# Kernel tuning notes

Measured on AMD Instinct MI355X. Metric: run time of the kernel, lower is better.

The kernel has to match this reference:

```python
import jax, jax.numpy as jnp
import numpy as np

N_HEAD = 12
NEG_INF = -10000.0


def setup_inputs() -> dict:
    key = jax.random.key(0)
    k1, k2, k3 = jax.random.split(key, 3)
    B, S, D = 8, 1024, 768
    std = 0.01
    return {
        "hidden_states": jax.random.normal(k1, (B, S, D), dtype=jnp.float32),
        "Wqkv": jax.random.normal(k2, (D, 3 * D), dtype=jnp.float32) * std,
        "bqkv": jnp.zeros((3 * D,), dtype=jnp.float32),
        "Wout": jax.random.normal(k3, (D, D), dtype=jnp.float32) * std,
        "bout": jnp.zeros((D,), dtype=jnp.float32),
    }


def reference(hidden_states, Wqkv, bqkv, Wout, bout):
    B, S, D = hidden_states.shape
    H = N_HEAD
    hd = D // H
    # fused QKV projection
    qkv = hidden_states @ Wqkv + bqkv  # [B,S,3D]
    qkv = qkv.reshape(B, S, 3, H, hd)
    q, k, v = qkv[:, :, 0], qkv[:, :, 1], qkv[:, :, 2]  # [B,S,H,hd]
    q = q.transpose(0, 2, 1, 3)  # [B,H,S,hd]
    k = k.transpose(0, 2, 1, 3)
    v = v.transpose(0, 2, 1, 3)
    scale = 1.0 / jnp.sqrt(jnp.asarray(hd, dtype=hidden_states.dtype))
    scores = jnp.einsum("bhqd,bhkd->bhqk", q, k) * scale  # [B,H,S,S]
    causal = jnp.tril(jnp.ones((S, S), dtype=bool))[None, None]
    scores = jnp.where(causal, scores, jnp.asarray(NEG_INF, scores.dtype))
    probs = jax.nn.softmax(scores, axis=-1)
    # dropout is identity in eval/deterministic mode
    attn = jnp.einsum("bhqk,bhkd->bhqd", probs, v)  # [B,H,S,hd]
    attn = attn.transpose(0, 2, 1, 3).reshape(B, S, D)
    return attn @ Wout + bout
```

## Files before the change

### kernel.cpp

```cpp
#include <hip/hip_runtime.h>
#include <hip/hip_bf16.h>

#define B_   8
#define S_   1024
#define D_   768
#define H_   12
#define HD_  64
#define BS_  (B_*S_)
#define N3_  (3*D_)

typedef __attribute__((ext_vector_type(8))) short short8;
typedef __attribute__((ext_vector_type(4))) float f32x4;

__device__ __forceinline__ short8 ld8(const __hip_bfloat16* p) {
    return *reinterpret_cast<const short8*>(p);
}
__device__ __forceinline__ void st8(__hip_bfloat16* p, short8 v) {
    *reinterpret_cast<short8*>(p) = v;
}
__device__ __forceinline__ f32x4 mfma16(short8 a, short8 b, f32x4 c) {
    return __builtin_amdgcn_mfma_f32_16x16x32_bf16(a, b, c, 0, 0, 0);
}
__device__ __forceinline__ void async16(const __hip_bfloat16* g, __hip_bfloat16* l) {
    __builtin_amdgcn_global_load_lds((const __attribute__((address_space(1))) void*)g,
                                     (__attribute__((address_space(3))) void*)l,
                                     16, 0, 0);
}
__device__ __forceinline__ float fast_exp2(float x) {
#if __has_builtin(__builtin_amdgcn_exp2f)
    return __builtin_amdgcn_exp2f(x);
#else
    return __expf(x * 0.69314718056f);
#endif
}

__global__ void cast_f32_bf16(const float* __restrict__ in,
                              __hip_bfloat16* __restrict__ out, int n) {
    int i = (blockIdx.x * blockDim.x + threadIdx.x) * 4;
    if (i + 3 < n) {
        float4 v = *reinterpret_cast<const float4*>(in + i);
        out[i + 0] = __float2bfloat16(v.x);
        out[i + 1] = __float2bfloat16(v.y);
        out[i + 2] = __float2bfloat16(v.z);
        out[i + 3] = __float2bfloat16(v.w);
    }
}

__global__ void transpose_cast(const float* __restrict__ in,
                               __hip_bfloat16* __restrict__ out, int R, int C) {
    __shared__ float tile[32][33];
    int c0 = blockIdx.x * 32, r0 = blockIdx.y * 32;
    for (int i = threadIdx.y; i < 32; i += 8) {
        tile[i][threadIdx.x] = in[(size_t)(r0 + i) * C + c0 + threadIdx.x];
    }
    __syncthreads();
    for (int i = threadIdx.y; i < 32; i += 8) {
        out[(size_t)(c0 + i) * R + r0 + threadIdx.x] =
            __float2bfloat16(tile[threadIdx.x][i]);
    }
}

__global__ __launch_bounds__(256)
void gemm_qkv(const __hip_bfloat16* __restrict__ A,
              const __hip_bfloat16* __restrict__ Bt,
              const float* __restrict__ bqkv,
              __hip_bfloat16* __restrict__ Qb,
              __hip_bfloat16* __restrict__ Kb,
              __hip_bfloat16* __restrict__ Vtb) {
    __shared__ __align__(16) char smem[49152];
    __hip_bfloat16* Ct = (__hip_bfloat16*)smem;

    int tid = threadIdx.x, wave = tid >> 6, lane = tid & 63;
    int ln = lane & 15, quad = lane >> 4;
    int mb = blockIdx.y * 128, nb = blockIdx.x * 128;
    int wm = (wave >> 1) * 64, wn = (wave & 1) * 64;

    f32x4 acc[4][4];
#pragma unroll
    for (int i = 0; i < 4; ++i)
#pragma unroll
        for (int j = 0; j < 4; ++j) acc[i][j] = (f32x4){0.f, 0.f, 0.f, 0.f};

    auto stage = [&](int k, int bufoff) {
        __hip_bfloat16* Asb = (__hip_bfloat16*)(smem + bufoff);
        __hip_bfloat16* Bsb = Asb + 128 * 32;
#pragma unroll
        for (int it = 0; it < 2; ++it) {
            int c = it * 256 + tid;
            int row = c >> 2, cc = c & 3;
            int csw = cc ^ ((row >> 1) & 3);
            async16(A + (size_t)(mb + row) * D_ + k + csw * 8,
                    Asb + it * 2048 + wave * 512);
            async16(Bt + (size_t)(nb + row) * D_ + k + csw * 8,
                    Bsb + it * 2048 + wave * 512);
        }
    };

    auto compute = [&](int bufoff) {
        __hip_bfloat16* As = (__hip_bfloat16*)(smem + bufoff);
        __hip_bfloat16* Bs = As + 128 * 32;
        short8 a[4], b[4];
#pragma unroll
        for (int i = 0; i < 4; ++i) {
            int row = wm + i * 16 + ln;
            a[i] = ld8(As + row * 32 + ((quad ^ ((row >> 1) & 3)) << 3));
        }
#pragma unroll
        for (int j = 0; j < 4; ++j) {
            int row = wn + j * 16 + ln;
            b[j] = ld8(Bs + row * 32 + ((quad ^ ((row >> 1) & 3)) << 3));
        }
#pragma unroll
        for (int i = 0; i < 4; ++i)
#pragma unroll
            for (int j = 0; j < 4; ++j)
                acc[i][j] = mfma16(a[i], b[j], acc[i][j]);
    };

    stage(0, 0);
    stage(32, 16384);
    int cb = 0;
    for (int k = 0; k < D_ - 32; k += 32) {
        asm volatile("s_waitcnt vmcnt(4)" ::: "memory");
        asm volatile("s_barrier" ::: "memory");
        if (k + 64 < D_) {
            int sb = cb + 32768; if (sb >= 49152) sb -= 49152;
            stage(k + 64, sb);
        }
        compute(cb);
        cb += 16384; if (cb >= 49152) cb = 0;
    }
    asm volatile("s_waitcnt vmcnt(0)" ::: "memory");
    asm volatile("s_barrier" ::: "memory");
    compute(cb);
    __syncthreads();

    int which = blockIdx.x / 6;
    int nbr = nb - which * D_;
    float qscale = (which == 0) ? (0.125f * 1.44269504089f) : 1.f;

#pragma unroll
    for (int j = 0; j < 4; ++j) {
        int col = wn + j * 16 + ln;
        float bias = bqkv[nb + col];
#pragma unroll
        for (int i = 0; i < 4; ++i)
#pragma unroll
            for (int r = 0; r < 4; ++r) {
                int row = wm + i * 16 + quad * 4 + r;
                __hip_bfloat16 v = __float2bfloat16((acc[i][j][r] + bias) * qscale);
                if (which != 2) Ct[row * 132 + col] = v;
                else            Ct[col * 132 + row] = v;
            }
    }
    __syncthreads();

    int bb = mb >> 10, sb = mb & 1023;
    if (which != 2) {
        __hip_bfloat16* dst = (which == 0) ? Qb : Kb;
#pragma unroll
        for (int it = 0; it < 8; ++it) {
            int cc = it * 256 + tid;
            int row = cc >> 4, c8 = cc & 15;
            short8 v = ld8(Ct + row * 132 + c8 * 8);
            int gcol = nbr + c8 * 8;
            int h = gcol >> 6, d = gcol & 63;
            int s = sb + row;
            st8(dst + (((size_t)(bb * H_ + h)) * S_ + s) * HD_ + d, v);
        }
    } else {
#pragma unroll
        for (int it = 0; it < 8; ++it) {
            int cc = it * 256 + tid;
            int drow = cc >> 4, s8 = cc & 15;
            short8 v = ld8(Ct + drow * 132 + s8 * 8);
            int gd = nbr + drow;
            int h = gd >> 6, d = gd & 63;
            st8(Vtb + ((size_t)(bb * H_ + h) * HD_ + d) * S_ + sb + s8 * 8, v);
        }
    }
}

__global__ __launch_bounds__(256, 3)
void attn_flash3(const __hip_bfloat16* __restrict__ Q,
                 const __hip_bfloat16* __restrict__ K,
                 const __hip_bfloat16* __restrict__ Vt,
                 __hip_bfloat16* __restrict__ attnbf) {
    __shared__ __hip_bfloat16 Kbuf[2][64 * 64];
    __shared__ __hip_bfloat16 Vbuf[2][64 * 64];
    __shared__ __hip_bfloat16 Pbuf[4][32 * 72];

    int bh = blockIdx.y;
    int ip = blockIdx.x;
    int tid = threadIdx.x;
    int wave = tid >> 6, lane = tid & 63;
    int ln = lane & 15, quad = lane >> 4;
    int strip = (wave < 2) ? ip : (15 - ip);
    int qrow0 = strip * 64 + (wave & 1) * 32;

    const __hip_bfloat16* Qbh = Q + (size_t)bh * S_ * HD_;
    const __hip_bfloat16* Kbh = K + (size_t)bh * S_ * HD_;
    const __hip_bfloat16* Vbh = Vt + (size_t)bh * HD_ * S_;

    short8 aq[2][2];
#pragma unroll
    for (int rt = 0; rt < 2; ++rt)
#pragma unroll
        for (int ks = 0; ks < 2; ++ks)
            aq[rt][ks] = ld8(Qbh + (size_t)(qrow0 + rt * 16 + ln) * HD_ +
                             ks * 32 + quad * 8);

    f32x4 o[2][4];
    float l_run[2][4];
#pragma unroll
    for (int rt = 0; rt < 2; ++rt)
#pragma unroll
        for (int n = 0; n < 4; ++n) {
            o[rt][n] = (f32x4){0.f, 0.f, 0.f, 0.f};
            l_run[rt][n] = 0.f;
        }

    int last_kt = 15 - ip;

    auto stage = [&](int kt, int buf) {
        const __hip_bfloat16* gK = Kbh + (size_t)kt * 64 * HD_;
#pragma unroll
        for (int it = 0; it < 2; ++it) {
            int p = it * 256 + tid;
            int row = p >> 3;
            int csw = (p & 7) ^ (row & 7);
            async16(gK + row * HD_ + csw * 8,
                    &Kbuf[buf][it * 2048 + wave * 512]);
            async16(Vbh + (size_t)row * S_ + kt * 64 + csw * 8,
                    &Vbuf[buf][it * 2048 + wave * 512]);
        }
    };

    stage(0, 0);
    __syncthreads();
    int cur = 0;

    for (int kt = 0; kt <= last_kt; ++kt) {
        int kbase = kt * 64;
        if (kt < last_kt) stage(kt + 1, cur ^ 1);

        if (kbase <= qrow0 + 31) {
            const __hip_bfloat16* Kc = Kbuf[cur];
            const __hip_bfloat16* Vc = Vbuf[cur];

            f32x4 s[2][4];
#pragma unroll
            for (int rt = 0; rt < 2; ++rt)
#pragma unroll
                for (int j = 0; j < 4; ++j) s[rt][j] = (f32x4){0.f, 0.f, 0.f, 0.f};
#pragma unroll
            for (int j = 0; j < 4; ++j) {
                int row = j * 16 + ln;
#pragma unroll
                for (int ks = 0; ks < 2; ++ks) {
                    short8 bk = ld8(&Kc[row * 64 +
                                        (((ks * 4 + quad) ^ (row & 7)) << 3)]);
#pragma unroll
                    for (int rt = 0; rt < 2; ++rt)
                        s[rt][j] = mfma16(aq[rt][ks], bk, s[rt][j]);
                }
            }

            if (kbase + 63 > qrow0) {
#pragma unroll
                for (int rt = 0; rt < 2; ++rt)
#pragma unroll
                    for (int j = 0; j < 4; ++j) {
                        int key = kbase + j * 16 + ln;
#pragma unroll
                        for (int r = 0; r < 4; ++r) {
                            int q = qrow0 + rt * 16 + quad * 4 + r;
                            if (key > q) s[rt][j][r] = -INFINITY;
                        }
                    }
            }

#pragma unroll
            for (int rt = 0; rt < 2; ++rt)
#pragma unroll
                for (int j = 0; j < 4; ++j)
#pragma unroll
                    for (int r = 0; r < 4; ++r)
                        s[rt][j][r] = fast_exp2(s[rt][j][r]);
#pragma unroll
            for (int rt = 0; rt < 2; ++rt)
#pragma unroll
                for (int r = 0; r < 4; ++r)
                    l_run[rt][r] += (s[rt][0][r] + s[rt][1][r]) +
                                    (s[rt][2][r] + s[rt][3][r]);

#pragma unroll
            for (int rt = 0; rt < 2; ++rt)
#pragma unroll
                for (int j = 0; j < 4; ++j)
#pragma unroll
                    for (int r = 0; r < 4; ++r)
                        Pbuf[wave][(rt * 16 + quad * 4 + r) * 72 + j * 16 + ln] =
                            __float2bfloat16(s[rt][j][r]);
            asm volatile("s_waitcnt lgkmcnt(0)" ::: "memory");

            short8 ap[2][2];
#pragma unroll
            for (int rt = 0; rt < 2; ++rt)
#pragma unroll
                for (int ks = 0; ks < 2; ++ks)
                    ap[rt][ks] = ld8(&Pbuf[wave][(rt * 16 + ln) * 72 +
                                                 ks * 32 + quad * 8]);

#pragma unroll
            for (int n = 0; n < 4; ++n) {
                int row = n * 16 + ln;
#pragma unroll
                for (int ks = 0; ks < 2; ++ks) {
                    short8 bv = ld8(&Vc[row * 64 +
                                        (((ks * 4 + quad) ^ (row & 7)) << 3)]);
#pragma unroll
                    for (int rt = 0; rt < 2; ++rt)
                        o[rt][n] = mfma16(ap[rt][ks], bv, o[rt][n]);
                }
            }
        }

        __syncthreads();
        cur ^= 1;
    }

    int bb = bh / H_, h = bh - bb * H_;
#pragma unroll
    for (int rt = 0; rt < 2; ++rt)
#pragma unroll
        for (int r = 0; r < 4; ++r) {
            float l = l_run[rt][r];
            l += __shfl_xor(l, 1);
            l += __shfl_xor(l, 2);
            l += __shfl_xor(l, 4);
            l += __shfl_xor(l, 8);
            float inv = 1.f / l;
            int row = qrow0 + rt * 16 + quad * 4 + r;
#pragma unroll
            for (int n = 0; n < 4; ++n) {
                int col = h * 64 + n * 16 + ln;
                attnbf[((size_t)bb * S_ + row) * D_ + col] =
                    __float2bfloat16(o[rt][n][r] * inv);
            }
        }
}

__global__ __launch_bounds__(256)
void gemm_out(const __hip_bfloat16* __restrict__ A,
              const __hip_bfloat16* __restrict__ Bt,
              const float* __restrict__ bias,
              float* __restrict__ Cout) {
    __shared__ __align__(16) char smem[49152];

    int tid = threadIdx.x, wave = tid >> 6, lane = tid & 63;
    int ln = lane & 15, quad = lane >> 4;
    int mb = blockIdx.y * 128, nb = blockIdx.x * 128;
    int wm = (wave >> 1) * 64, wn = (wave & 1) * 64;

    f32x4 acc[4][4];
#pragma unroll
    for (int i = 0; i < 4; ++i)
#pragma unroll
        for (int j = 0; j < 4; ++j) acc[i][j] = (f32x4){0.f, 0.f, 0.f, 0.f};

    auto stage = [&](int k, int bufoff) {
        __hip_bfloat16* Asb = (__hip_bfloat16*)(smem + bufoff);
        __hip_bfloat16* Bsb = Asb + 128 * 32;
#pragma unroll
        for (int it = 0; it < 2; ++it) {
            int c = it * 256 + tid;
            int row = c >> 2, cc = c & 3;
            int csw = cc ^ ((row >> 1) & 3);
            async16(A + (size_t)(mb + row) * D_ + k + csw * 8,
                    Asb + it * 2048 + wave * 512);
            async16(Bt + (size_t)(nb + row) * D_ + k + csw * 8,
                    Bsb + it * 2048 + wave * 512);
        }
    };

    auto compute = [&](int bufoff) {
        __hip_bfloat16* As = (__hip_bfloat16*)(smem + bufoff);
        __hip_bfloat16* Bs = As + 128 * 32;
        short8 a[4], b[4];
#pragma unroll
        for (int i = 0; i < 4; ++i) {
            int row = wm + i * 16 + ln;
            a[i] = ld8(As + row * 32 + ((quad ^ ((row >> 1) & 3)) << 3));
        }
#pragma unroll
        for (int j = 0; j < 4; ++j) {
            int row = wn + j * 16 + ln;
            b[j] = ld8(Bs + row * 32 + ((quad ^ ((row >> 1) & 3)) << 3));
        }
#pragma unroll
        for (int i = 0; i < 4; ++i)
#pragma unroll
            for (int j = 0; j < 4; ++j)
                acc[i][j] = mfma16(a[i], b[j], acc[i][j]);
    };

    stage(0, 0);
    stage(32, 16384);
    int cb = 0;
    for (int k = 0; k < D_ - 32; k += 32) {
        asm volatile("s_waitcnt vmcnt(4)" ::: "memory");
        asm volatile("s_barrier" ::: "memory");
        if (k + 64 < D_) {
            int sb = cb + 32768; if (sb >= 49152) sb -= 49152;
            stage(k + 64, sb);
        }
        compute(cb);
        cb += 16384; if (cb >= 49152) cb = 0;
    }
    asm volatile("s_waitcnt vmcnt(0)" ::: "memory");
    asm volatile("s_barrier" ::: "memory");
    compute(cb);

#pragma unroll
    for (int j = 0; j < 4; ++j) {
        int col = nb + wn + j * 16 + ln;
        float bv = bias[col];
#pragma unroll
        for (int i = 0; i < 4; ++i)
#pragma unroll
            for (int r = 0; r < 4; ++r) {
                int row = mb + wm + i * 16 + quad * 4 + r;
                Cout[(size_t)row * D_ + col] = acc[i][j][r] + bv;
            }
    }
}

extern "C" void kernel_launch(void* const* d_in, const int* in_sizes, int n_in,
                              void* d_out, int out_size, void* d_ws, size_t ws_size,
                              hipStream_t stream) {
    const float* X    = (const float*)d_in[0];
    const float* Wqkv = (const float*)d_in[1];
    const float* bqkv = (const float*)d_in[2];
    const float* Wout = (const float*)d_in[3];
    const float* bout = (const float*)d_in[4];
    float* out = (float*)d_out;

    constexpr size_t SZ_XBF   = (size_t)BS_ * D_ * 2;
    constexpr size_t SZ_WQKVT = (size_t)N3_ * D_ * 2;
    constexpr size_t SZ_WOUTT = (size_t)D_ * D_ * 2;
    constexpr size_t SZ_QKV   = (size_t)B_ * H_ * S_ * HD_ * 2;

    char* w = (char*)d_ws;
    __hip_bfloat16* Xbf    = (__hip_bfloat16*)(w);
    __hip_bfloat16* WqkvT  = (__hip_bfloat16*)(w + SZ_XBF);
    __hip_bfloat16* WoutT  = (__hip_bfloat16*)(w + SZ_XBF + SZ_WQKVT);
    __hip_bfloat16* Qb     = (__hip_bfloat16*)(w + SZ_XBF + SZ_WQKVT + SZ_WOUTT);
    __hip_bfloat16* Kb     = (__hip_bfloat16*)(w + SZ_XBF + SZ_WQKVT + SZ_WOUTT + SZ_QKV);
    __hip_bfloat16* Vtb    = (__hip_bfloat16*)(w + SZ_XBF + SZ_WQKVT + SZ_WOUTT + 2*SZ_QKV);
    __hip_bfloat16* attnbf = (__hip_bfloat16*)(w + SZ_XBF + SZ_WQKVT + SZ_WOUTT + 3*SZ_QKV);
    (void)ws_size; (void)in_sizes; (void)n_in; (void)out_size;

    int nX = BS_ * D_;
    cast_f32_bf16<<<nX / (256 * 4), 256, 0, stream>>>(X, Xbf, nX);
    transpose_cast<<<dim3(N3_ / 32, D_ / 32), dim3(32, 8), 0, stream>>>(Wqkv, WqkvT, D_, N3_);
    transpose_cast<<<dim3(D_ / 32, D_ / 32), dim3(32, 8), 0, stream>>>(Wout, WoutT, D_, D_);

    gemm_qkv<<<dim3(N3_ / 128, BS_ / 128), 256, 0, stream>>>(Xbf, WqkvT, bqkv, Qb, Kb, Vtb);

    attn_flash3<<<dim3(8, B_ * H_), 256, 0, stream>>>(Qb, Kb, Vtb, attnbf);

    gemm_out<<<dim3(D_ / 128, BS_ / 128), 256, 0, stream>>>(attnbf, WoutT, bout, out);
}
```

Measured before the change: 191.1 us.

## Merge prep kernels, remap GEMM block order, narrow out-proj tile to 64 columns

Folds the X cast and both weight transposes into a single prep launch, removing two kernel launches and their gaps. Both GEMMs remap block indices so that consecutive launched blocks are spread across the M dimension in groups of 8, aiming for better cache or XCD locality. The output projection drops from 128x128 to 128x64 tiles, doubling its grid from 384 to 768 blocks so more CUs stay busy on MI355X, at the cost of lower per-block reuse. LDS buffering and the waitcnt values are adjusted to match.

```diff
diff --git a/kernel.cpp b/kernel.cpp
--- a/kernel.cpp
+++ b/kernel.cpp
@@ -34,30 +34,41 @@
 #endif
 }
 
-__global__ void cast_f32_bf16(const float* __restrict__ in,
-                              __hip_bfloat16* __restrict__ out, int n) {
-    int i = (blockIdx.x * blockDim.x + threadIdx.x) * 4;
-    if (i + 3 < n) {
-        float4 v = *reinterpret_cast<const float4*>(in + i);
-        out[i + 0] = __float2bfloat16(v.x);
-        out[i + 1] = __float2bfloat16(v.y);
-        out[i + 2] = __float2bfloat16(v.z);
-        out[i + 3] = __float2bfloat16(v.w);
-    }
-}
-
-__global__ void transpose_cast(const float* __restrict__ in,
-                               __hip_bfloat16* __restrict__ out, int R, int C) {
+#define PREP_CAST_BLK 6144
+#define PREP_WQKV_BLK 1728
+#define PREP_WOUT_BLK 576
+__global__ __launch_bounds__(256)
+void prep(const float* __restrict__ X, __hip_bfloat16* __restrict__ Xbf,
+          const float* __restrict__ Wqkv, __hip_bfloat16* __restrict__ WqkvT,
+          const float* __restrict__ Wout, __hip_bfloat16* __restrict__ WoutT) {
     __shared__ float tile[32][33];
-    int c0 = blockIdx.x * 32, r0 = blockIdx.y * 32;
-    for (int i = threadIdx.y; i < 32; i += 8) {
-        tile[i][threadIdx.x] = in[(size_t)(r0 + i) * C + c0 + threadIdx.x];
-    }
+    int b = blockIdx.x, tid = threadIdx.x;
+    if (b < PREP_CAST_BLK) {
+        int i = (b * 256 + tid) * 4;
+        float4 v = *reinterpret_cast<const float4*>(X + i);
+        Xbf[i + 0] = __float2bfloat16(v.x);
+        Xbf[i + 1] = __float2bfloat16(v.y);
+        Xbf[i + 2] = __float2bfloat16(v.z);
+        Xbf[i + 3] = __float2bfloat16(v.w);
+        return;
+    }
+    const float* in; __hip_bfloat16* out; int Rr, Cc, bx, by;
+    if (b < PREP_CAST_BLK + PREP_WQKV_BLK) {
+        int sub = b - PREP_CAST_BLK;
+        bx = sub % (N3_ / 32); by = sub / (N3_ / 32);
+        in = Wqkv; out = WqkvT; Rr = D_; Cc = N3_;
+    } else {
+        int sub = b - PREP_CAST_BLK - PREP_WQKV_BLK;
+        bx = sub % (D_ / 32); by = sub / (D_ / 32);
+        in = Wout; out = WoutT; Rr = D_; Cc = D_;
+    }
+    int tx = tid & 31, ty = tid >> 5;
+    int c0 = bx * 32, r0 = by * 32;
+    for (int i = ty; i < 32; i += 8)
+        tile[i][tx] = in[(size_t)(r0 + i) * Cc + c0 + tx];
     __syncthreads();
-    for (int i = threadIdx.y; i < 32; i += 8) {
-        out[(size_t)(c0 + i) * R + r0 + threadIdx.x] =
-            __float2bfloat16(tile[threadIdx.x][i]);
-    }
+    for (int i = ty; i < 32; i += 8)
+        out[(size_t)(c0 + i) * Rr + r0 + tx] = __float2bfloat16(tile[tx][i]);
 }
 
 __global__ __launch_bounds__(256)
@@ -72,7 +83,10 @@
 
     int tid = threadIdx.x, wave = tid >> 6, lane = tid & 63;
     int ln = lane & 15, quad = lane >> 4;
-    int mb = blockIdx.y * 128, nb = blockIdx.x * 128;
+    int lin = blockIdx.y * 18 + blockIdx.x;
+    int work = (lin & 7) * 144 + (lin >> 3);
+    int mbb = work / 18, nbb = work % 18;
+    int mb = mbb * 128, nb = nbb * 128;
     int wm = (wave >> 1) * 64, wn = (wave & 1) * 64;
 
     f32x4 acc[4][4];
@@ -135,7 +149,7 @@
     compute(cb);
     __syncthreads();
 
-    int which = blockIdx.x / 6;
+    int which = nbb / 6;
     int nbr = nb - which * D_;
     float qscale = (which == 0) ? (0.125f * 1.44269504089f) : 1.f;
 
@@ -356,18 +370,21 @@
               const __hip_bfloat16* __restrict__ Bt,
               const float* __restrict__ bias,
               float* __restrict__ Cout) {
-    __shared__ __align__(16) char smem[49152];
+    __shared__ __align__(16) char smem[36864];
 
     int tid = threadIdx.x, wave = tid >> 6, lane = tid & 63;
     int ln = lane & 15, quad = lane >> 4;
-    int mb = blockIdx.y * 128, nb = blockIdx.x * 128;
-    int wm = (wave >> 1) * 64, wn = (wave & 1) * 64;
-
-    f32x4 acc[4][4];
+    int lin = blockIdx.y * 12 + blockIdx.x;
+    int work = (lin & 7) * 96 + (lin >> 3);
+    int mbb = work / 12, nbb = work % 12;
+    int mb = mbb * 128, nb = nbb * 64;
+    int wm = (wave >> 1) * 64, wn = (wave & 1) * 32;
+
+    f32x4 acc[4][2];
 #pragma unroll
     for (int i = 0; i < 4; ++i)
 #pragma unroll
-        for (int j = 0; j < 4; ++j) acc[i][j] = (f32x4){0.f, 0.f, 0.f, 0.f};
+        for (int j = 0; j < 2; ++j) acc[i][j] = (f32x4){0.f, 0.f, 0.f, 0.f};
 
     auto stage = [&](int k, int bufoff) {
         __hip_bfloat16* Asb = (__hip_bfloat16*)(smem + bufoff);
@@ -379,51 +396,56 @@
             int csw = cc ^ ((row >> 1) & 3);
             async16(A + (size_t)(mb + row) * D_ + k + csw * 8,
                     Asb + it * 2048 + wave * 512);
+        }
+        {
+            int c = tid;
+            int row = c >> 2, cc = c & 3;
+            int csw = cc ^ ((row >> 1) & 3);
             async16(Bt + (size_t)(nb + row) * D_ + k + csw * 8,
-                    Bsb + it * 2048 + wave * 512);
+                    Bsb + wave * 512);
         }
     };
 
     auto compute = [&](int bufoff) {
         __hip_bfloat16* As = (__hip_bfloat16*)(smem + bufoff);
         __hip_bfloat16* Bs = As + 128 * 32;
-        short8 a[4], b[4];
+        short8 a[4], b[2];
 #pragma unroll
         for (int i = 0; i < 4; ++i) {
             int row = wm + i * 16 + ln;
             a[i] = ld8(As + row * 32 + ((quad ^ ((row >> 1) & 3)) << 3));
         }
 #pragma unroll
-        for (int j = 0; j < 4; ++j) {
+        for (int j = 0; j < 2; ++j) {
             int row = wn + j * 16 + ln;
             b[j] = ld8(Bs + row * 32 + ((quad ^ ((row >> 1) & 3)) << 3));
         }
 #pragma unroll
         for (int i = 0; i < 4; ++i)
 #pragma unroll
-            for (int j = 0; j < 4; ++j)
+            for (int j = 0; j < 2; ++j)
                 acc[i][j] = mfma16(a[i], b[j], acc[i][j]);
     };
 
     stage(0, 0);
-    stage(32, 16384);
+    stage(32, 12288);
     int cb = 0;
     for (int k = 0; k < D_ - 32; k += 32) {
-        asm volatile("s_waitcnt vmcnt(4)" ::: "memory");
+        asm volatile("s_waitcnt vmcnt(3)" ::: "memory");
         asm volatile("s_barrier" ::: "memory");
         if (k + 64 < D_) {
-            int sb = cb + 32768; if (sb >= 49152) sb -= 49152;
+            int sb = cb + 24576; if (sb >= 36864) sb -= 36864;
             stage(k + 64, sb);
         }
         compute(cb);
-        cb += 16384; if (cb >= 49152) cb = 0;
+        cb += 12288; if (cb >= 36864) cb = 0;
     }
     asm volatile("s_waitcnt vmcnt(0)" ::: "memory");
     asm volatile("s_barrier" ::: "memory");
     compute(cb);
 
 #pragma unroll
-    for (int j = 0; j < 4; ++j) {
+    for (int j = 0; j < 2; ++j) {
         int col = nb + wn + j * 16 + ln;
         float bv = bias[col];
 #pragma unroll
@@ -461,14 +483,12 @@
     __hip_bfloat16* attnbf = (__hip_bfloat16*)(w + SZ_XBF + SZ_WQKVT + SZ_WOUTT + 3*SZ_QKV);
     (void)ws_size; (void)in_sizes; (void)n_in; (void)out_size;
 
-    int nX = BS_ * D_;
-    cast_f32_bf16<<<nX / (256 * 4), 256, 0, stream>>>(X, Xbf, nX);
-    transpose_cast<<<dim3(N3_ / 32, D_ / 32), dim3(32, 8), 0, stream>>>(Wqkv, WqkvT, D_, N3_);
-    transpose_cast<<<dim3(D_ / 32, D_ / 32), dim3(32, 8), 0, stream>>>(Wout, WoutT, D_, D_);
+    prep<<<PREP_CAST_BLK + PREP_WQKV_BLK + PREP_WOUT_BLK, 256, 0, stream>>>(
+        X, Xbf, Wqkv, WqkvT, Wout, WoutT);
 
     gemm_qkv<<<dim3(N3_ / 128, BS_ / 128), 256, 0, stream>>>(Xbf, WqkvT, bqkv, Qb, Kb, Vtb);
 
     attn_flash3<<<dim3(8, B_ * H_), 256, 0, stream>>>(Qb, Kb, Vtb, attnbf);
 
-    gemm_out<<<dim3(D_ / 128, BS_ / 128), 256, 0, stream>>>(attnbf, WoutT, bout, out);
-}
+    gemm_out<<<dim3(D_ / 64, BS_ / 128), 256, 0, stream>>>(attnbf, WoutT, bout, out);
+}
```

New measurement: 183.6 us. 3.9% less time.
